# Kernel tuning notes

Hardware: AMD Instinct MI355X
Metric: run time of the kernel (lower is better)

The kernel has to match this reference:

```python
import jax, jax.numpy as jnp
import numpy as np

A = 4096      # alleles
RPA = 20      # mean reads per allele
R = A * RPA   # total reads per data source
C = 12        # input channels (pileup features)
L = 32        # read window length
D = 32        # hidden feature dim
NOUT = 2


def setup_inputs() -> dict:
    key = jax.random.key(0)
    k = jax.random.split(key, 8)
    # ragged read counts per allele (alternating 16/24, mean 20, sums to R)
    counts0 = np.tile(np.array([16, 24], dtype=np.int64), A // 2)
    counts1 = np.tile(np.array([24, 16], dtype=np.int64), A // 2)
    return {
        "tensors0": jax.random.normal(k[0], (R, C, L), dtype=jnp.float32),
        "tensors1": jax.random.normal(k[1], (R, C, L), dtype=jnp.float32),
        "W0": jax.random.normal(k[2], (D, C), dtype=jnp.float32) * 0.1,
        "b0": jnp.zeros((D,), dtype=jnp.float32),
        "W1": jax.random.normal(k[3], (D, C), dtype=jnp.float32) * 0.1,
        "b1": jnp.zeros((D,), dtype=jnp.float32),
        "W2": jax.random.normal(k[4], (NOUT, 2 * D), dtype=jnp.float32) * 0.1,
        "b2": jnp.zeros((NOUT,), dtype=jnp.float32),
        "numReadsPerAllele0": jnp.asarray(counts0),
        "numReadsPerAllele1": jnp.asarray(counts1),
        "numAllelesPerSite": jnp.full((A // 2,), 2, dtype=jnp.int64),
        "depthMultiplier0": jnp.asarray(counts0, dtype=jnp.float32),
        "depthMultiplier1": jnp.asarray(counts1, dtype=jnp.float32),
    }


def _frames(t, W, b):
    # pointwise read-feature extractor: [R,C,L] -> [R,D,L]
    return jax.nn.relu(jnp.einsum('rcl,dc->rdl', t, W) + b[None, :, None])


def reference(tensors0, tensors1, W0, b0, W1, b1, W2, b2,
              numReadsPerAllele0, numReadsPerAllele1,
              numAllelesPerSite, depthMultiplier0, depthMultiplier1):
    nA = numReadsPerAllele0.shape[0]
    nR = tensors0.shape[0]
    # segment ids replace torch.split + per-segment torch.sum (ragged segment-sum)
    seg0 = jnp.repeat(jnp.arange(nA), numReadsPerAllele0, total_repeat_length=nR)
    seg1 = jnp.repeat(jnp.arange(nA), numReadsPerAllele1, total_repeat_length=nR)

    frames0 = _frames(tensors0, W0, b0)  # [R,D,L]
    frames1 = _frames(tensors1, W1, b1)

    red0 = jax.ops.segment_sum(frames0, seg0, num_segments=nA)  # [A,D,L]
    red1 = jax.ops.segment_sum(frames1, seg1, num_segments=nA)

    # depth normalization (normalize() in the original)
    red0 = red0 / depthMultiplier0[:, None, None]
    red1 = red1 / depthMultiplier1[:, None, None]

    reduced = jnp.concatenate((red0, red1), axis=1)  # [A, 2D, L]

    # network2 (GraphSearcher): site-specific head modeled as pool + linear
    pooled = jnp.mean(reduced, axis=2)               # [A, 2D]
    return pooled @ W2.T + b2                        # [A, NOUT]
```

## Files before the change

### kernel.cpp

```cpp
#include <hip/hip_runtime.h>

#define A_ALLELES 4096
#define CCH 12
#define LW 32
#define DH 32
#define RDF (CCH * LW)

typedef __attribute__((ext_vector_type(8)))  short bf16x8;
typedef __attribute__((ext_vector_type(16))) float f32x16;

__device__ inline unsigned pk2(float fa, float fb) {
    const unsigned a = __float_as_uint(fa), b = __float_as_uint(fb);
    return ((a + 0x8000u) >> 16) | ((b + 0x8000u) & 0xffff0000u);
}

__global__ __launch_bounds__(256) void scan_kernel(
    const int* __restrict__ c0, const int* __restrict__ c1,
    int* __restrict__ o0, int* __restrict__ o1)
{
    const int* c = (blockIdx.x == 0) ? c0 : c1;
    int*       o = (blockIdx.x == 0) ? o0 : o1;

    __shared__ int part[256];
    const int tid  = threadIdx.x;
    const int base = tid * 16;

    int loc[16];
    int s = 0;
#pragma unroll
    for (int i = 0; i < 16; ++i) { loc[i] = c[base + i]; s += loc[i]; }
    part[tid] = s;
    __syncthreads();

    for (int st = 1; st < 256; st <<= 1) {
        int v = (tid >= st) ? part[tid - st] : 0;
        __syncthreads();
        part[tid] += v;
        __syncthreads();
    }

    int excl = (tid == 0) ? 0 : part[tid - 1];
#pragma unroll
    for (int i = 0; i < 16; ++i) { o[base + i] = excl; excl += loc[i]; }
}

__global__ __launch_bounds__(256, 4) void main_kernel(
    const float* __restrict__ t0, const float* __restrict__ t1,
    const float* __restrict__ W0, const float* __restrict__ b0,
    const float* __restrict__ W1, const float* __restrict__ b1,
    const float* __restrict__ W2, const float* __restrict__ b2,
    const int*  __restrict__ cnt0, const int* __restrict__ cnt1,
    const float* __restrict__ dm0, const float* __restrict__ dm1,
    const int*  __restrict__ offs0, const int* __restrict__ offs1,
    float* __restrict__ out)
{
    __shared__ float sW2[2 * 2 * DH];
    __shared__ float sB2[2];

    const int tid = threadIdx.x;
    if (tid < 2 * 2 * DH) sW2[tid] = W2[tid];
    if (tid < 2) sB2[tid] = b2[tid];
    __syncthreads();

    const int w    = tid >> 6;
    const int lane = tid & 63;
    const int src  = blockIdx.x >> 10;
    const int a    = ((blockIdx.x & 1023) << 2) | w;

    const float* __restrict__ tens = src ? t1 : t0;
    const int*   __restrict__ cnt  = src ? cnt1 : cnt0;
    const int*   __restrict__ offs = src ? offs1 : offs0;
    const float* __restrict__ dm   = src ? dm1 : dm0;
    const float* __restrict__ gW   = src ? W1 : W0;
    const float* __restrict__ gB   = src ? b1 : b0;

    const int l = lane & 31;
    const int h = lane >> 5;

    union { bf16x8 v; unsigned u[4]; } Af;
#pragma unroll
    for (int p = 0; p < 4; ++p) {
        const int c0 = h * 8 + 2 * p, c1 = c0 + 1;
        const float f0 = (c0 < CCH) ? gW[l * CCH + c0] : 0.f;
        const float f1 = (c1 < CCH) ? gW[l * CCH + c1] : 0.f;
        Af.u[p] = pk2(f0, f1);
    }
    f32x16 cb;
#pragma unroll
    for (int reg = 0; reg < 16; ++reg)
        cb[reg] = gB[(reg & 3) + 8 * (reg >> 2) + 4 * h];

    const int n     = cnt[a];
    const int start = offs[a];
    const float* rb = tens + (size_t)start * RDF;

    const float* pLo = rb + l + h * 256;
    const float* pHi = rb + l + (h ? 256 : 128);

    float acc[16];
#pragma unroll
    for (int reg = 0; reg < 16; ++reg) acc[reg] = 0.f;

#define LOAD8(buf, P, W_)  do {                                     \
        buf[0] = pLo[(P) + 0];  buf[1] = pLo[(P) + 32];             \
        buf[2] = pLo[(P) + 64]; buf[3] = pLo[(P) + 96];             \
        buf[4] = pHi[(P) + 0];  buf[5] = pHi[(P) + 32];             \
        buf[6] = pHi[(P) + 64]; buf[7] = pHi[(P) + 96]; } while (0)

#define PACK_MFMA_ACC(buf) do {                                     \
        union { bf16x8 v; unsigned u[4]; } Bf;                      \
        Bf.u[0] = pk2(buf[0], buf[1]); Bf.u[1] = pk2(buf[2], buf[3]); \
        Bf.u[2] = pk2(buf[4], buf[5]); Bf.u[3] = pk2(buf[6], buf[7]); \
        const f32x16 D = __builtin_amdgcn_mfma_f32_32x32x16_bf16(   \
            Af.v, Bf.v, cb, 0, 0, 0);                               \
        _Pragma("unroll")                                           \
        for (int reg = 0; reg < 16; ++reg)                          \
            acc[reg] += fmaxf(D[reg], 0.f); } while (0)

    const int n2 = n & ~1;
    if (n2 >= 2) {
        float bA[8], bB[8];
        LOAD8(bA, 0, 0);
        LOAD8(bB, 384, 0);
        const int iters = (n2 - 2) >> 1;
        for (int it = 0; it < iters; ++it) {
            {
                union { bf16x8 v; unsigned u[4]; } Bf;
                Bf.u[0] = pk2(bA[0], bA[1]); Bf.u[1] = pk2(bA[2], bA[3]);
                Bf.u[2] = pk2(bA[4], bA[5]); Bf.u[3] = pk2(bA[6], bA[7]);
                LOAD8(bA, 768, 0);
                const f32x16 D = __builtin_amdgcn_mfma_f32_32x32x16_bf16(
                    Af.v, Bf.v, cb, 0, 0, 0);
#pragma unroll
                for (int reg = 0; reg < 16; ++reg) acc[reg] += fmaxf(D[reg], 0.f);
                pLo += 384; pHi += 384;
            }
            {
                union { bf16x8 v; unsigned u[4]; } Bf;
                Bf.u[0] = pk2(bB[0], bB[1]); Bf.u[1] = pk2(bB[2], bB[3]);
                Bf.u[2] = pk2(bB[4], bB[5]); Bf.u[3] = pk2(bB[6], bB[7]);
                LOAD8(bB, 768, 0);
                const f32x16 D = __builtin_amdgcn_mfma_f32_32x32x16_bf16(
                    Af.v, Bf.v, cb, 0, 0, 0);
#pragma unroll
                for (int reg = 0; reg < 16; ++reg) acc[reg] += fmaxf(D[reg], 0.f);
                pLo += 384; pHi += 384;
            }
        }
        PACK_MFMA_ACC(bA);
        PACK_MFMA_ACC(bB);
    }
    if (n & 1) {
        const float* qLo = rb + (size_t)(n - 1) * RDF + l + h * 256;
        const float* qHi = rb + (size_t)(n - 1) * RDF + l + (h ? 256 : 128);
        float bT[8];
        bT[0] = qLo[0];  bT[1] = qLo[32]; bT[2] = qLo[64]; bT[3] = qLo[96];
        bT[4] = qHi[0];  bT[5] = qHi[32]; bT[6] = qHi[64]; bT[7] = qHi[96];
        PACK_MFMA_ACC(bT);
    }

#pragma unroll
    for (int reg = 0; reg < 16; ++reg) {
#pragma unroll
        for (int mm = 1; mm < 32; mm <<= 1)
            acc[reg] += __shfl_xor(acc[reg], mm, 64);
    }

    const float scale = 1.f / (32.f * dm[a]);
    float c0s = 0.f, c1s = 0.f;
#pragma unroll
    for (int reg = 0; reg < 16; ++reg) {
        const int d = (reg & 3) + 8 * (reg >> 2) + 4 * h;
        const float pv = acc[reg] * scale;
        c0s = fmaf(pv, sW2[0 * 2 * DH + src * DH + d], c0s);
        c1s = fmaf(pv, sW2[1 * 2 * DH + src * DH + d], c1s);
    }
    c0s += __shfl_xor(c0s, 32, 64);
    c1s += __shfl_xor(c1s, 32, 64);

    if (lane == 0) {
        if (src == 0) { c0s += sB2[0]; c1s += sB2[1]; }
        atomicAdd(&out[a * 2 + 0], c0s);
        atomicAdd(&out[a * 2 + 1], c1s);
    }
#undef LOAD8
#undef PACK_MFMA_ACC
}

extern "C" void kernel_launch(void* const* d_in, const int* in_sizes, int n_in,
                              void* d_out, int out_size, void* d_ws, size_t ws_size,
                              hipStream_t stream) {
    const float* t0  = (const float*)d_in[0];
    const float* t1  = (const float*)d_in[1];
    const float* W0  = (const float*)d_in[2];
    const float* b0  = (const float*)d_in[3];
    const float* W1  = (const float*)d_in[4];
    const float* b1  = (const float*)d_in[5];
    const float* W2  = (const float*)d_in[6];
    const float* b2  = (const float*)d_in[7];
    const int*  cnt0 = (const int*)d_in[8];
    const int*  cnt1 = (const int*)d_in[9];
    const float* dm0 = (const float*)d_in[11];
    const float* dm1 = (const float*)d_in[12];

    int* offs0 = (int*)d_ws;
    int* offs1 = offs0 + A_ALLELES;

    hipMemsetAsync(d_out, 0, (size_t)out_size * sizeof(float), stream);
    scan_kernel<<<2, 256, 0, stream>>>(cnt0, cnt1, offs0, offs1);

    main_kernel<<<2048, 256, 0, stream>>>(
        t0, t1, W0, b0, W1, b1, W2, b2,
        cnt0, cnt1, dm0, dm1, offs0, offs1, (float*)d_out);
}
```

Baseline: 295.2 us.

## Stage read pairs through LDS with async global_load_lds triple buffering

Replaces the strided per-lane scalar global loads with 16-byte-per-lane async global-to-LDS copies of whole read pairs into a per-wave 3-slot ring, gated by explicit vmcnt waits. The kernel then reads its MFMA operands from LDS and runs two MFMAs per pair. The aim is wider, coalesced global transactions and deeper prefetch to raise memory bandwidth in this bandwidth-bound kernel. In exchange it uses about 36KB of LDS per block, which may lower occupancy, and it depends on hand-written waitcnt correctness with no wave barrier between the async writes and the LDS reads.

Result: no change. 297.2 us (+0.7%).

```diff
diff --git a/kernel.cpp b/kernel.cpp
--- a/kernel.cpp
+++ b/kernel.cpp
@@ -5,6 +5,8 @@
 #define LW 32
 #define DH 32
 #define RDF (CCH * LW)
+#define PAIRF (2 * RDF)
+#define NSLOT 3
 
 typedef __attribute__((ext_vector_type(8)))  short bf16x8;
 typedef __attribute__((ext_vector_type(16))) float f32x16;
@@ -12,6 +14,12 @@
 __device__ inline unsigned pk2(float fa, float fb) {
     const unsigned a = __float_as_uint(fa), b = __float_as_uint(fb);
     return ((a + 0x8000u) >> 16) | ((b + 0x8000u) & 0xffff0000u);
+}
+
+__device__ inline void gld16(const float* g, float* lds) {
+    __builtin_amdgcn_global_load_lds(
+        (const __attribute__((address_space(1))) void*)g,
+        (__attribute__((address_space(3))) void*)lds, 16, 0, 0);
 }
 
 __global__ __launch_bounds__(256) void scan_kernel(
@@ -54,6 +62,7 @@
     const int*  __restrict__ offs0, const int* __restrict__ offs1,
     float* __restrict__ out)
 {
+    __shared__ float stage[4][NSLOT][PAIRF];
     __shared__ float sW2[2 * 2 * DH];
     __shared__ float sB2[2];
 
@@ -94,69 +103,73 @@
     const int start = offs[a];
     const float* rb = tens + (size_t)start * RDF;
 
-    const float* pLo = rb + l + h * 256;
-    const float* pHi = rb + l + (h ? 256 : 128);
+    const int lane4 = lane * 4;
+
+    const int ldsLo = h * 8 * LW + l;
+    const int ldsHi = (h ? 8 : 4) * LW + l;
 
     float acc[16];
 #pragma unroll
     for (int reg = 0; reg < 16; ++reg) acc[reg] = 0.f;
 
-#define LOAD8(buf, P, W_)  do {                                     \
-        buf[0] = pLo[(P) + 0];  buf[1] = pLo[(P) + 32];             \
-        buf[2] = pLo[(P) + 64]; buf[3] = pLo[(P) + 96];             \
-        buf[4] = pHi[(P) + 0];  buf[5] = pHi[(P) + 32];             \
-        buf[6] = pHi[(P) + 64]; buf[7] = pHi[(P) + 96]; } while (0)
-
-#define PACK_MFMA_ACC(buf) do {                                     \
-        union { bf16x8 v; unsigned u[4]; } Bf;                      \
-        Bf.u[0] = pk2(buf[0], buf[1]); Bf.u[1] = pk2(buf[2], buf[3]); \
-        Bf.u[2] = pk2(buf[4], buf[5]); Bf.u[3] = pk2(buf[6], buf[7]); \
-        const f32x16 D = __builtin_amdgcn_mfma_f32_32x32x16_bf16(   \
-            Af.v, Bf.v, cb, 0, 0, 0);                               \
-        _Pragma("unroll")                                           \
-        for (int reg = 0; reg < 16; ++reg)                          \
-            acc[reg] += fmaxf(D[reg], 0.f); } while (0)
-
-    const int n2 = n & ~1;
-    if (n2 >= 2) {
-        float bA[8], bB[8];
-        LOAD8(bA, 0, 0);
-        LOAD8(bB, 384, 0);
-        const int iters = (n2 - 2) >> 1;
-        for (int it = 0; it < iters; ++it) {
-            {
-                union { bf16x8 v; unsigned u[4]; } Bf;
-                Bf.u[0] = pk2(bA[0], bA[1]); Bf.u[1] = pk2(bA[2], bA[3]);
-                Bf.u[2] = pk2(bA[4], bA[5]); Bf.u[3] = pk2(bA[6], bA[7]);
-                LOAD8(bA, 768, 0);
-                const f32x16 D = __builtin_amdgcn_mfma_f32_32x32x16_bf16(
-                    Af.v, Bf.v, cb, 0, 0, 0);
-#pragma unroll
-                for (int reg = 0; reg < 16; ++reg) acc[reg] += fmaxf(D[reg], 0.f);
-                pLo += 384; pHi += 384;
-            }
-            {
-                union { bf16x8 v; unsigned u[4]; } Bf;
-                Bf.u[0] = pk2(bB[0], bB[1]); Bf.u[1] = pk2(bB[2], bB[3]);
-                Bf.u[2] = pk2(bB[4], bB[5]); Bf.u[3] = pk2(bB[6], bB[7]);
-                LOAD8(bB, 768, 0);
-                const f32x16 D = __builtin_amdgcn_mfma_f32_32x32x16_bf16(
-                    Af.v, Bf.v, cb, 0, 0, 0);
-#pragma unroll
-                for (int reg = 0; reg < 16; ++reg) acc[reg] += fmaxf(D[reg], 0.f);
-                pLo += 384; pHi += 384;
-            }
+#define STAGE_PAIR(slot, pr) do {                                     \
+        const float* g_ = rb + (size_t)(pr) * PAIRF + lane4;          \
+        gld16(g_,       &stage[w][slot][0]);                          \
+        gld16(g_ + 256, &stage[w][slot][256]);                        \
+        gld16(g_ + 512, &stage[w][slot][512]);  } while (0)
+
+#define READ8_PACK(ptr, Bf) do {                                      \
+        float v0 = (ptr)[ldsLo +  0], v1 = (ptr)[ldsLo + 32];         \
+        float v2 = (ptr)[ldsLo + 64], v3 = (ptr)[ldsLo + 96];         \
+        float v4 = (ptr)[ldsHi +  0], v5 = (ptr)[ldsHi + 32];         \
+        float v6 = (ptr)[ldsHi + 64], v7 = (ptr)[ldsHi + 96];         \
+        Bf.u[0] = pk2(v0, v1); Bf.u[1] = pk2(v2, v3);                 \
+        Bf.u[2] = pk2(v4, v5); Bf.u[3] = pk2(v6, v7); } while (0)
+
+    const int P = n >> 1;
+    if (P > 0) {
+        STAGE_PAIR(0, 0);
+        STAGE_PAIR(1, (P > 1) ? 1 : 0);
+
+        int s = 0;
+        for (int p = 0; p < P; ++p) {
+            const int rp = (p + 2 < P) ? (p + 2) : (P - 1);
+            int sp = s + 2; if (sp >= NSLOT) sp -= NSLOT;
+            STAGE_PAIR(sp, rp);
+
+            asm volatile("s_waitcnt vmcnt(6)" ::: "memory");
+
+            const float* s0 = &stage[w][s][0];
+            const float* s1 = s0 + RDF;
+
+            union { bf16x8 v; unsigned u[4]; } Bf0, Bf1;
+            READ8_PACK(s0, Bf0);
+            READ8_PACK(s1, Bf1);
+
+            const f32x16 D0 = __builtin_amdgcn_mfma_f32_32x32x16_bf16(
+                Af.v, Bf0.v, cb, 0, 0, 0);
+            const f32x16 D1 = __builtin_amdgcn_mfma_f32_32x32x16_bf16(
+                Af.v, Bf1.v, cb, 0, 0, 0);
+#pragma unroll
+            for (int reg = 0; reg < 16; ++reg)
+                acc[reg] += fmaxf(D0[reg], 0.f) + fmaxf(D1[reg], 0.f);
+
+            ++s; if (s >= NSLOT) s = 0;
         }
-        PACK_MFMA_ACC(bA);
-        PACK_MFMA_ACC(bB);
     }
     if (n & 1) {
-        const float* qLo = rb + (size_t)(n - 1) * RDF + l + h * 256;
-        const float* qHi = rb + (size_t)(n - 1) * RDF + l + (h ? 256 : 128);
-        float bT[8];
-        bT[0] = qLo[0];  bT[1] = qLo[32]; bT[2] = qLo[64]; bT[3] = qLo[96];
-        bT[4] = qHi[0];  bT[5] = qHi[32]; bT[6] = qHi[64]; bT[7] = qHi[96];
-        PACK_MFMA_ACC(bT);
+        const float* q = rb + (size_t)(n - 1) * RDF;
+        float v0 = q[ldsLo +  0], v1 = q[ldsLo + 32];
+        float v2 = q[ldsLo + 64], v3 = q[ldsLo + 96];
+        float v4 = q[ldsHi +  0], v5 = q[ldsHi + 32];
+        float v6 = q[ldsHi + 64], v7 = q[ldsHi + 96];
+        union { bf16x8 v; unsigned u[4]; } Bf;
+        Bf.u[0] = pk2(v0, v1); Bf.u[1] = pk2(v2, v3);
+        Bf.u[2] = pk2(v4, v5); Bf.u[3] = pk2(v6, v7);
+        const f32x16 D = __builtin_amdgcn_mfma_f32_32x32x16_bf16(
+            Af.v, Bf.v, cb, 0, 0, 0);
+#pragma unroll
+        for (int reg = 0; reg < 16; ++reg) acc[reg] += fmaxf(D[reg], 0.f);
     }
 
 #pragma unroll
@@ -183,8 +196,8 @@
         atomicAdd(&out[a * 2 + 0], c0s);
         atomicAdd(&out[a * 2 + 1], c1s);
     }
-#undef LOAD8
-#undef PACK_MFMA_ACC
+#undef STAGE_PAIR
+#undef READ8_PACK
 }
 
 extern "C" void kernel_launch(void* const* d_in, const int* in_sizes, int n_in,
```

## Split ragged allele segments into fixed 8-read chunks with a work table

Applied to the files above, without the earlier changes.

The scan kernel now builds a per-source table of chunk records (allele id, first-chunk flag, length up to 8, start read), and each wave of the main kernel processes one chunk instead of one whole allele. Full chunks issue all eight reads' loads up front before doing the MFMAs, which raises memory-level parallelism and evens out the load imbalance between 16- and 24-read alleles. In exchange there are more atomic adds per allele, more waves, a longer serial scan, and a fixed grid sized for the maximum chunk count, with surplus waves exiting early.

Result: slower. 341.3 us (+15.6%).

```diff
diff --git a/kernel.cpp b/kernel.cpp
--- a/kernel.cpp
+++ b/kernel.cpp
@@ -5,6 +5,9 @@
 #define LW 32
 #define DH 32
 #define RDF (CCH * LW)
+#define CHK 8
+#define MAXCH 14336
+#define NBH 3584
 
 typedef __attribute__((ext_vector_type(8)))  short bf16x8;
 typedef __attribute__((ext_vector_type(16))) float f32x16;
@@ -16,32 +19,53 @@
 
 __global__ __launch_bounds__(256) void scan_kernel(
     const int* __restrict__ c0, const int* __restrict__ c1,
-    int* __restrict__ o0, int* __restrict__ o1)
+    int2* __restrict__ tbl0, int2* __restrict__ tbl1,
+    int* __restrict__ nch)
 {
-    const int* c = (blockIdx.x == 0) ? c0 : c1;
-    int*       o = (blockIdx.x == 0) ? o0 : o1;
-
-    __shared__ int part[256];
+    const int sidx = blockIdx.x;
+    const int* __restrict__ c = sidx == 0 ? c0 : c1;
+    int2* __restrict__ tbl = sidx == 0 ? tbl0 : tbl1;
+
+    __shared__ int partR[256], partC[256];
     const int tid  = threadIdx.x;
     const int base = tid * 16;
 
     int loc[16];
-    int s = 0;
-#pragma unroll
-    for (int i = 0; i < 16; ++i) { loc[i] = c[base + i]; s += loc[i]; }
-    part[tid] = s;
+    int s = 0, sc = 0;
+#pragma unroll
+    for (int i = 0; i < 16; ++i) {
+        loc[i] = c[base + i];
+        s += loc[i];
+        sc += (loc[i] + CHK - 1) / CHK;
+    }
+    partR[tid] = s; partC[tid] = sc;
     __syncthreads();
 
     for (int st = 1; st < 256; st <<= 1) {
-        int v = (tid >= st) ? part[tid - st] : 0;
+        int vr = (tid >= st) ? partR[tid - st] : 0;
+        int vc = (tid >= st) ? partC[tid - st] : 0;
         __syncthreads();
-        part[tid] += v;
+        partR[tid] += vr; partC[tid] += vc;
         __syncthreads();
     }
 
-    int excl = (tid == 0) ? 0 : part[tid - 1];
-#pragma unroll
-    for (int i = 0; i < 16; ++i) { o[base + i] = excl; excl += loc[i]; }
+    int exR = tid ? partR[tid - 1] : 0;
+    int exC = tid ? partC[tid - 1] : 0;
+#pragma unroll
+    for (int i = 0; i < 16; ++i) {
+        const int n = loc[i];
+        int first = 0x80;
+        for (int j = 0; j < n; j += CHK) {
+            int len = n - j; if (len > CHK) len = CHK;
+            int2 rec;
+            rec.x = ((base + i) << 8) | first | len;
+            rec.y = exR + j;
+            tbl[exC++] = rec;
+            first = 0;
+        }
+        exR += n;
+    }
+    if (tid == 255) nch[sidx] = partC[255];
 }
 
 __global__ __launch_bounds__(256, 4) void main_kernel(
@@ -49,9 +73,9 @@
     const float* __restrict__ W0, const float* __restrict__ b0,
     const float* __restrict__ W1, const float* __restrict__ b1,
     const float* __restrict__ W2, const float* __restrict__ b2,
-    const int*  __restrict__ cnt0, const int* __restrict__ cnt1,
     const float* __restrict__ dm0, const float* __restrict__ dm1,
-    const int*  __restrict__ offs0, const int* __restrict__ offs1,
+    const int2* __restrict__ tbl0, const int2* __restrict__ tbl1,
+    const int* __restrict__ nch,
     float* __restrict__ out)
 {
     __shared__ float sW2[2 * 2 * DH];
@@ -64,12 +88,18 @@
 
     const int w    = tid >> 6;
     const int lane = tid & 63;
-    const int src  = blockIdx.x >> 10;
-    const int a    = ((blockIdx.x & 1023) << 2) | w;
+    const int src  = (blockIdx.x >= NBH) ? 1 : 0;
+    const int ci   = (blockIdx.x - src * NBH) * 4 + w;
+
+    if (ci >= nch[src]) return;
+
+    const int2 rec = (src ? tbl1 : tbl0)[ci];
+    const int a         = rec.x >> 8;
+    const int len       = rec.x & 0x7f;
+    const int firstChnk = rec.x & 0x80;
+    const int startRead = rec.y;
 
     const float* __restrict__ tens = src ? t1 : t0;
-    const int*   __restrict__ cnt  = src ? cnt1 : cnt0;
-    const int*   __restrict__ offs = src ? offs1 : offs0;
     const float* __restrict__ dm   = src ? dm1 : dm0;
     const float* __restrict__ gW   = src ? W1 : W0;
     const float* __restrict__ gB   = src ? b1 : b0;
@@ -90,74 +120,61 @@
     for (int reg = 0; reg < 16; ++reg)
         cb[reg] = gB[(reg & 3) + 8 * (reg >> 2) + 4 * h];
 
-    const int n     = cnt[a];
-    const int start = offs[a];
-    const float* rb = tens + (size_t)start * RDF;
-
-    const float* pLo = rb + l + h * 256;
-    const float* pHi = rb + l + (h ? 256 : 128);
+    const float* rb = tens + (size_t)startRead * RDF;
+    const int offLo = h * 8 * LW + l;
+    const int offHi = (h ? 8 : 4) * LW + l;
 
     float acc[16];
 #pragma unroll
     for (int reg = 0; reg < 16; ++reg) acc[reg] = 0.f;
 
-#define LOAD8(buf, P, W_)  do {                                     \
-        buf[0] = pLo[(P) + 0];  buf[1] = pLo[(P) + 32];             \
-        buf[2] = pLo[(P) + 64]; buf[3] = pLo[(P) + 96];             \
-        buf[4] = pHi[(P) + 0];  buf[5] = pHi[(P) + 32];             \
-        buf[6] = pHi[(P) + 64]; buf[7] = pHi[(P) + 96]; } while (0)
-
-#define PACK_MFMA_ACC(buf) do {                                     \
-        union { bf16x8 v; unsigned u[4]; } Bf;                      \
-        Bf.u[0] = pk2(buf[0], buf[1]); Bf.u[1] = pk2(buf[2], buf[3]); \
-        Bf.u[2] = pk2(buf[4], buf[5]); Bf.u[3] = pk2(buf[6], buf[7]); \
-        const f32x16 D = __builtin_amdgcn_mfma_f32_32x32x16_bf16(   \
-            Af.v, Bf.v, cb, 0, 0, 0);                               \
-        _Pragma("unroll")                                           \
-        for (int reg = 0; reg < 16; ++reg)                          \
+#define PACK_MFMA_ACC(vv) do {                                        \
+        union { bf16x8 v; unsigned u[4]; } Bf;                        \
+        Bf.u[0] = pk2(vv[0], vv[1]); Bf.u[1] = pk2(vv[2], vv[3]);     \
+        Bf.u[2] = pk2(vv[4], vv[5]); Bf.u[3] = pk2(vv[6], vv[7]);     \
+        const f32x16 D = __builtin_amdgcn_mfma_f32_32x32x16_bf16(     \
+            Af.v, Bf.v, cb, 0, 0, 0);                                 \
+        _Pragma("unroll")                                             \
+        for (int reg = 0; reg < 16; ++reg)                            \
             acc[reg] += fmaxf(D[reg], 0.f); } while (0)
 
-    const int n2 = n & ~1;
-    if (n2 >= 2) {
-        float bA[8], bB[8];
-        LOAD8(bA, 0, 0);
-        LOAD8(bB, 384, 0);
-        const int iters = (n2 - 2) >> 1;
-        for (int it = 0; it < iters; ++it) {
-            {
-                union { bf16x8 v; unsigned u[4]; } Bf;
-                Bf.u[0] = pk2(bA[0], bA[1]); Bf.u[1] = pk2(bA[2], bA[3]);
-                Bf.u[2] = pk2(bA[4], bA[5]); Bf.u[3] = pk2(bA[6], bA[7]);
-                LOAD8(bA, 768, 0);
-                const f32x16 D = __builtin_amdgcn_mfma_f32_32x32x16_bf16(
-                    Af.v, Bf.v, cb, 0, 0, 0);
-#pragma unroll
-                for (int reg = 0; reg < 16; ++reg) acc[reg] += fmaxf(D[reg], 0.f);
-                pLo += 384; pHi += 384;
+    if (len == CHK) {
+        float va[4][8], vb[4][8];
+#pragma unroll
+        for (int rr = 0; rr < 4; ++rr) {
+            const float* p = rb + rr * RDF;
+#pragma unroll
+            for (int j = 0; j < 4; ++j) {
+                va[rr][j]     = p[offLo + j * 32];
+                va[rr][4 + j] = p[offHi + j * 32];
             }
-            {
-                union { bf16x8 v; unsigned u[4]; } Bf;
-                Bf.u[0] = pk2(bB[0], bB[1]); Bf.u[1] = pk2(bB[2], bB[3]);
-                Bf.u[2] = pk2(bB[4], bB[5]); Bf.u[3] = pk2(bB[6], bB[7]);
-                LOAD8(bB, 768, 0);
-                const f32x16 D = __builtin_amdgcn_mfma_f32_32x32x16_bf16(
-                    Af.v, Bf.v, cb, 0, 0, 0);
-#pragma unroll
-                for (int reg = 0; reg < 16; ++reg) acc[reg] += fmaxf(D[reg], 0.f);
-                pLo += 384; pHi += 384;
+        }
+#pragma unroll
+        for (int rr = 0; rr < 4; ++rr) {
+            const float* p = rb + (4 + rr) * RDF;
+#pragma unroll
+            for (int j = 0; j < 4; ++j) {
+                vb[rr][j]     = p[offLo + j * 32];
+                vb[rr][4 + j] = p[offHi + j * 32];
             }
         }
-        PACK_MFMA_ACC(bA);
-        PACK_MFMA_ACC(bB);
-    }
-    if (n & 1) {
-        const float* qLo = rb + (size_t)(n - 1) * RDF + l + h * 256;
-        const float* qHi = rb + (size_t)(n - 1) * RDF + l + (h ? 256 : 128);
-        float bT[8];
-        bT[0] = qLo[0];  bT[1] = qLo[32]; bT[2] = qLo[64]; bT[3] = qLo[96];
-        bT[4] = qHi[0];  bT[5] = qHi[32]; bT[6] = qHi[64]; bT[7] = qHi[96];
-        PACK_MFMA_ACC(bT);
-    }
+#pragma unroll
+        for (int rr = 0; rr < 4; ++rr) PACK_MFMA_ACC(va[rr]);
+#pragma unroll
+        for (int rr = 0; rr < 4; ++rr) PACK_MFMA_ACC(vb[rr]);
+    } else {
+        for (int rr = 0; rr < len; ++rr) {
+            const float* p = rb + (size_t)rr * RDF;
+            float vv[8];
+#pragma unroll
+            for (int j = 0; j < 4; ++j) {
+                vv[j]     = p[offLo + j * 32];
+                vv[4 + j] = p[offHi + j * 32];
+            }
+            PACK_MFMA_ACC(vv);
+        }
+    }
+#undef PACK_MFMA_ACC
 
 #pragma unroll
     for (int reg = 0; reg < 16; ++reg) {
@@ -179,12 +196,10 @@
     c1s += __shfl_xor(c1s, 32, 64);
 
     if (lane == 0) {
-        if (src == 0) { c0s += sB2[0]; c1s += sB2[1]; }
+        if (src == 0 && firstChnk) { c0s += sB2[0]; c1s += sB2[1]; }
         atomicAdd(&out[a * 2 + 0], c0s);
         atomicAdd(&out[a * 2 + 1], c1s);
     }
-#undef LOAD8
-#undef PACK_MFMA_ACC
 }
 
 extern "C" void kernel_launch(void* const* d_in, const int* in_sizes, int n_in,
@@ -203,13 +218,14 @@
     const float* dm0 = (const float*)d_in[11];
     const float* dm1 = (const float*)d_in[12];
 
-    int* offs0 = (int*)d_ws;
-    int* offs1 = offs0 + A_ALLELES;
+    int*  nch  = (int*)d_ws;
+    int2* tbl0 = (int2*)((char*)d_ws + 16);
+    int2* tbl1 = tbl0 + MAXCH;
 
     hipMemsetAsync(d_out, 0, (size_t)out_size * sizeof(float), stream);
-    scan_kernel<<<2, 256, 0, stream>>>(cnt0, cnt1, offs0, offs1);
-
-    main_kernel<<<2048, 256, 0, stream>>>(
+    scan_kernel<<<2, 256, 0, stream>>>(cnt0, cnt1, tbl0, tbl1, nch);
+
+    main_kernel<<<2 * NBH, 256, 0, stream>>>(
         t0, t1, W0, b0, W1, b1, W2, b2,
-        cnt0, cnt1, dm0, dm1, offs0, offs1, (float*)d_out);
-}
+        dm0, dm1, tbl0, tbl1, nch, (float*)d_out);
+}
```
